# Performance work log

Measured on AMD Instinct MI355X. Metric: run time of the kernel, lower is better.

The kernel has to match this reference:

```python
import jax, jax.numpy as jnp
import numpy as np
import math

BS, SEQ, LQ = 64, 2048, 128
NHEADS, D_TIME, NH, DV = 4, 128, 128, 2
D_K = D_TIME // NHEADS
T10_LO, T10_HI = 0.1, 5.0
M0_LO, M0_HI = 0.1, 10.0
XFA_MAX_DEG = 25.0
REG_H = 200


def setup_inputs() -> dict:
    key = jax.random.key(0)
    ks = jax.random.split(key, 40)
    w = lambda i, shape, s=0.05: jax.random.normal(ks[i], shape, dtype=jnp.float32) * s
    return {
        "X_fa_in": jax.random.uniform(ks[0], (BS, SEQ), dtype=jnp.float32),
        "fa_vals": jax.random.uniform(ks[1], (BS, SEQ), dtype=jnp.float32),
        "fa_mask": jax.random.bernoulli(ks[2], 0.7, (BS, SEQ)),
        "fa_len": jnp.full((BS, 1), float(SEQ), dtype=jnp.float32),
        "TR_vals": jax.random.uniform(ks[3], (BS, SEQ), dtype=jnp.float32),
        "te_lin_w": w(4, (1, 1)), "te_lin_b": w(5, (1,)),
        "te_per_w": w(6, (D_TIME - 1, 1), 1.0), "te_per_b": w(7, (D_TIME - 1,)),
        "q_w": w(8, (D_TIME, D_TIME)), "q_b": w(9, (D_TIME,)),
        "k_w": w(10, (D_TIME, D_TIME)), "k_b": w(11, (D_TIME,)),
        "att_out_w": w(12, (NH, NHEADS * DV)), "att_out_b": w(13, (NH,)),
        "gru_wih": w(14, (3 * NH, NH)), "gru_whh": w(15, (3 * NH, NH)),
        "gru_bih": w(16, (3 * NH,)), "gru_bhh": w(17, (3 * NH,)),
        "score_t10_w": w(18, (1, NH)), "score_m0_w": w(19, (1, NH)),
        "regT_w1": w(20, (REG_H, NH)), "regT_b1": w(21, (REG_H,)),
        "regT_w2": w(22, (REG_H, REG_H)), "regT_b2": w(23, (REG_H,)),
        "regT_w3": w(24, (1, REG_H)), "regT_b3": w(25, (1,)),
        "regM_w1": w(26, (REG_H, NH)), "regM_b1": w(27, (REG_H,)),
        "regM_w2": w(28, (REG_H, REG_H)), "regM_b2": w(29, (REG_H,)),
        "regM_w3": w(30, (1, REG_H)), "regM_b3": w(31, (1,)),
    }


def _time_embed(t, lw, lb, pw, pb):
    # t: (..., L) -> (..., L, D_TIME); linear(1->1) concat sin(linear(1->D_TIME-1))
    t = t[..., None]
    lin = t * lw[0, 0] + lb                      # (..., L, 1)
    per = jnp.sin(t @ pw.T + pb)                 # (..., L, D_TIME-1)
    return jnp.concatenate([lin, per], axis=-1)


def _gru(x, wih, whh, bih, bhh):
    # x: (bs, T, NH) -> (bs, T, NH), torch nn.GRU semantics, h0 = 0
    x_gates = jnp.einsum('bth,gh->btg', x, wih) + bih  # (bs, T, 3*NH)

    def step(h, xt):
        gh = h @ whh.T + bhh
        ri, zi, ni = jnp.split(xt, 3, axis=-1)
        rh, zh, nh = jnp.split(gh, 3, axis=-1)
        r = jax.nn.sigmoid(ri + rh)
        z = jax.nn.sigmoid(zi + zh)
        n = jnp.tanh(ni + r * nh)
        hn = (1.0 - z) * n + z * h
        return hn, hn

    h0 = jnp.zeros((x.shape[0], whh.shape[1]), dtype=x.dtype)
    _, hs = jax.lax.scan(step, h0, x_gates.transpose(1, 0, 2))
    return hs.transpose(1, 0, 2)


def _mlp(h, w1, b1, w2, b2, w3, b3):
    h = jax.nn.gelu(h @ w1.T + b1, approximate=False)
    h = jax.nn.gelu(h @ w2.T + b2, approximate=False)
    return h @ w3.T + b3


def reference(X_fa_in, fa_vals, fa_mask, fa_len, TR_vals,
              te_lin_w, te_lin_b, te_per_w, te_per_b,
              q_w, q_b, k_w, k_b, att_out_w, att_out_b,
              gru_wih, gru_whh, gru_bih, gru_bhh,
              score_t10_w, score_m0_w,
              regT_w1, regT_b1, regT_w2, regT_b2, regT_w3, regT_b3,
              regM_w1, regM_b1, regM_w2, regM_b2, regM_w3, regM_b3):
    bs, seq = X_fa_in.shape
    # ---- time embeddings (dropout inactive / eval) ----
    key_input = fa_vals / math.radians(XFA_MAX_DEG - 1.0)
    k_emb = _time_embed(key_input, te_lin_w, te_lin_b, te_per_w, te_per_b)   # (bs, seq, D_TIME)
    q_ref = jnp.linspace(0.0, 1.0, LQ, dtype=X_fa_in.dtype)[None, :]         # (1, LQ)
    q_emb = _time_embed(q_ref, te_lin_w, te_lin_b, te_per_w, te_per_b)       # (1, LQ, D_TIME)

    # ---- multi-time attention ----
    q = (q_emb @ q_w.T + q_b).reshape(1, LQ, NHEADS, D_K).transpose(0, 2, 1, 3)[0]  # (h, LQ, d_k)
    k = (k_emb @ k_w.T + k_b).reshape(bs, seq, NHEADS, D_K).transpose(0, 2, 1, 3)    # (bs, h, seq, d_k)
    scores = jnp.einsum('hqd,bhsd->bhqs', q, k) / jnp.sqrt(jnp.asarray(D_K, X_fa_in.dtype))
    # mask is broadcast identically across the d_v replication in the original,
    # so the per-channel softmax collapses to one softmax over keys.
    scores = jnp.where(fa_mask[:, None, None, :], scores, jnp.asarray(-1e9, scores.dtype))
    p = jax.nn.softmax(scores, axis=-1)                                      # (bs, h, LQ, seq)
    v = jnp.concatenate([X_fa_in[..., None], fa_mask.astype(X_fa_in.dtype)[..., None]], axis=-1)  # (bs, seq, 2)
    attn = jnp.einsum('bhqs,bsd->bhqd', p, v)                                # (bs, h, LQ, 2)
    concat = attn.transpose(0, 2, 1, 3).reshape(bs, LQ, NHEADS * DV)
    att_out = concat @ att_out_w.T + att_out_b                               # (bs, LQ, NH)

    # ---- GRU + attention pooling ----
    out = _gru(att_out, gru_wih, gru_whh, gru_bih, gru_bhh)                  # (bs, LQ, NH)
    sT = jax.nn.softmax(out @ score_t10_w.T, axis=1)                         # (bs, LQ, 1)
    sM = jax.nn.softmax(out @ score_m0_w.T, axis=1)
    hidden_T10 = jnp.sum(out * sT, axis=1)                                   # (bs, NH)
    hidden_M0 = jnp.sum(out * sM, axis=1)

    T10 = T10_LO + jax.nn.sigmoid(_mlp(hidden_T10, regT_w1, regT_b1, regT_w2, regT_b2, regT_w3, regT_b3)) * (T10_HI - T10_LO)  # (bs, 1)
    M0 = M0_LO + jax.nn.sigmoid(_mlp(hidden_M0, regM_w1, regM_b1, regM_w2, regM_b2, regM_w3, regM_b3)) * (M0_HI - M0_LO)       # (bs, 1)
    R1 = 1.0 / T10
    E = jnp.exp(-TR_vals * R1)                                               # (bs, seq)
    X_out = (1.0 - E) * jnp.sin(fa_vals) / (1.0 - jnp.cos(fa_vals) * E) * M0
    return (X_out, T10, M0)
```

## Files before the change

kernel.cpp:

```cpp
#include <hip/hip_runtime.h>

#define BS 64
#define SEQ 2048
#define LQ 128
#define NH 128

typedef short bf16x8 __attribute__((ext_vector_type(8)));
typedef float f32x4 __attribute__((ext_vector_type(4)));
typedef unsigned short u16x4 __attribute__((ext_vector_type(4)));
typedef unsigned uint2v __attribute__((ext_vector_type(2)));

__device__ __forceinline__ unsigned short f2bf(float f) {
  unsigned u = __float_as_uint(f);
  u = (u + 0x7FFFu + ((u >> 16) & 1u)) >> 16;
  return (unsigned short)u;
}
__device__ __forceinline__ float b2f(unsigned short u) {
  return __uint_as_float((unsigned)u << 16);
}
__device__ __forceinline__ float sigm(float x) { return 1.f / (1.f + __expf(-x)); }
__device__ __forceinline__ float gelu_f(float x) { return 0.5f * x * (1.f + erff(x * 0.70710678118654752f)); }
__device__ __forceinline__ float fexp2(float x) { float y; asm("v_exp_f32 %0, %1" : "=v"(y) : "v"(x)); return y; }
__device__ __forceinline__ float frcp(float x) { float y; asm("v_rcp_f32 %0, %1" : "=v"(y) : "v"(x)); return y; }
__device__ __forceinline__ unsigned cvtpk(float lo, float hi) {
  unsigned d; asm("v_cvt_pk_bf16_f32 %0, %1, %2" : "=v"(d) : "v"(lo), "v"(hi)); return d;
}

__device__ __forceinline__ void softbar() {
  asm volatile("s_waitcnt lgkmcnt(0)" ::: "memory");
  __builtin_amdgcn_s_barrier();
  __builtin_amdgcn_sched_barrier(0);
}

__global__ __launch_bounds__(384) void k_prep(
    const void* __restrict__ mraw,
    const float* __restrict__ qw, const float* __restrict__ qb,
    const float* __restrict__ lw, const float* __restrict__ lb,
    const float* __restrict__ pw, const float* __restrict__ pb,
    const float* __restrict__ wih, const float* __restrict__ bih,
    const float* __restrict__ bhh,
    const float* __restrict__ aow, const float* __restrict__ aob,
    float* __restrict__ maskf, unsigned short* __restrict__ qbf,
    float* __restrict__ fwc) {
  const int tid = threadIdx.x;
  const int blk = blockIdx.x;
  if (blk < 342) {
    __shared__ int sflag;
    if (tid < 64) {
      const unsigned* raw = (const unsigned*)mraw;
      int isf = 0, isb = 0;
#pragma unroll
      for (int k = 0; k < 4; ++k) {
        unsigned w = raw[tid + k * 64];
        isf |= (w == 0x3F800000u);
        isb |= (w > 1u);
      }
      isf = __any(isf);
      isb = __any(isb);
      if (tid == 0) sflag = isf ? 2 : (isb ? 1 : 0);
    }
    __syncthreads();
    int fl = sflag;
    int i = blk * 384 + tid;
    if (i < BS * SEQ) {
      float v;
      if (fl == 2)      v = (((const float*)mraw)[i] != 0.f) ? 1.f : 0.f;
      else if (fl == 1) v = (((const unsigned char*)mraw)[i] != 0) ? 1.f : 0.f;
      else              v = (((const int*)mraw)[i] != 0) ? 1.f : 0.f;
      maskf[i] = v;
    }
  } else if (blk < 350) {
    __shared__ float emb[16 * 132];
    __shared__ float Ac[128], Bc[128];
    const int sb = blk - 342;
    if (tid < 128) {
      Ac[tid] = (tid == 0) ? lw[0] : pw[tid - 1];
      Bc[tid] = (tid == 0) ? lb[0] : pb[tid - 1];
    }
    __syncthreads();
    if (tid < 256) {
      int lq = tid >> 4, e0 = (tid & 15) * 8;
      float tv = (float)(sb * 16 + lq) * (1.f / 127.f);
#pragma unroll
      for (int k = 0; k < 8; ++k) {
        int e = e0 + k;
        float arg = fmaf(tv, Ac[e], Bc[e]);
        emb[lq * 132 + e] = (e == 0) ? arg : __sinf(arg);
      }
    }
    __syncthreads();
    if (tid < 256) {
      const int c = tid & 127, lh = tid >> 7;
      float acc[8];
#pragma unroll
      for (int i = 0; i < 8; ++i) acc[i] = qb[c];
      for (int e4 = 0; e4 < 32; ++e4) {
        float4 wv = *(const float4*)(qw + c * 128 + e4 * 4);
#pragma unroll
        for (int i = 0; i < 8; ++i) {
          const float* er = &emb[(lh * 8 + i) * 132 + e4 * 4];
          acc[i] += wv.x * er[0] + wv.y * er[1] + wv.z * er[2] + wv.w * er[3];
        }
      }
#pragma unroll
      for (int i = 0; i < 8; ++i) {
        int lq = sb * 16 + lh * 8 + i;
        qbf[((c >> 5) * LQ + lq) * 32 + (c & 31)] = f2bf(acc[i]);
      }
    }
  } else {
    const int g = tid;
    const float sc = (g < 256) ? -1.4426950408889634f : 2.8853900817779268f;
    float fw[8];
#pragma unroll
    for (int c = 0; c < 8; ++c) fw[c] = 0.f;
    float cg = bih[g] + (g < 256 ? bhh[g] : 0.f);
    for (int j = 0; j < 128; ++j) {
      float w = wih[g * 128 + j];
      cg = fmaf(w, aob[j], cg);
#pragma unroll
      for (int c = 0; c < 8; ++c) fw[c] = fmaf(w, aow[j * 8 + c], fw[c]);
    }
#pragma unroll
    for (int c = 0; c < 8; ++c) fwc[g * 12 + c] = fw[c] * sc;
    fwc[g * 12 + 8] = cg * sc;
  }
}

__global__ __launch_bounds__(384) void k_xgate(
    const float* __restrict__ fwc, const float* __restrict__ part,
    unsigned short* __restrict__ xg) {
  __shared__ float at[64][8];
  const int tid = threadIdx.x;
  const int t = blockIdx.x;
  if (tid < 256) {
    int b = tid >> 2, h = tid & 3;
    const float* p = part + ((size_t)(b * LQ + t) * 4 + h) * 8;
    float4 p0 = *(const float4*)p;
    float4 p1 = *(const float4*)(p + 4);
    float a = p0.x + p0.z + p1.x + p1.z;
    float l = p0.y + p0.w + p1.y + p1.w;
    at[b][h * 2] = a / l;
    at[b][h * 2 + 1] = 1.f;
  }
  __syncthreads();
  const int q = tid >> 2, s = tid & 3;
  float wv[4][8], cg[4];
#pragma unroll
  for (int j = 0; j < 4; ++j) {
    int row = q * 4 + j;
    float4 a0 = *(const float4*)(fwc + row * 12);
    float4 a1 = *(const float4*)(fwc + row * 12 + 4);
    wv[j][0] = a0.x; wv[j][1] = a0.y; wv[j][2] = a0.z; wv[j][3] = a0.w;
    wv[j][4] = a1.x; wv[j][5] = a1.y; wv[j][6] = a1.z; wv[j][7] = a1.w;
    cg[j] = fwc[row * 12 + 8];
  }
  unsigned short* obase = xg + (((size_t)t * 96 + q) * 64 + s * 16) * 4;
#pragma unroll 4
  for (int bb = 0; bb < 16; ++bb) {
    const float* a = at[s * 16 + bb];
    u16x4 o;
#pragma unroll
    for (int j = 0; j < 4; ++j) {
      float acc = cg[j] + wv[j][0] * a[0] + wv[j][1] * a[1] + wv[j][2] * a[2] + wv[j][3] * a[3]
                        + wv[j][4] * a[4] + wv[j][5] * a[5] + wv[j][6] * a[6] + wv[j][7] * a[7];
      o[j] = f2bf(acc);
    }
    *(u16x4*)(obase + bb * 4) = o;
  }
}

__global__ __launch_bounds__(256) void k_attn(
    const float* __restrict__ Xfa, const float* __restrict__ maskf,
    const float* __restrict__ fav,
    const float* __restrict__ kw, const float* __restrict__ kb,
    const float* __restrict__ lw, const float* __restrict__ lb,
    const float* __restrict__ pw, const float* __restrict__ pb,
    const unsigned short* __restrict__ qbf,
    float* __restrict__ part) {
  __shared__ unsigned short kwl[128 * 136];
  __shared__ unsigned short ktl[64 * 136];
  __shared__ float xt[64], mtl[64], kbl[128], Ac[128], Bc[128];

  const int tid = threadIdx.x;
  const int lane = tid & 63, wave = tid >> 6;
  const int l15 = lane & 15, kg = lane >> 4;
  const int b = blockIdx.x >> 2, qt = blockIdx.x & 3;
  const float KSCALE = 2.3873241463784303f;
  const float C2 = 0.25505654f;

  if (tid < 128) {
    Ac[tid] = (tid == 0) ? lw[0] : pw[tid - 1];
    Bc[tid] = (tid == 0) ? lb[0] : pb[tid - 1];
    kbl[tid] = kb[tid];
  }
  for (int idx = tid; idx < 2048; idx += 256) {
    int d = idx >> 4, e0 = (idx & 15) * 8;
    const float* src = kw + d * 128 + e0;
    float4 s0 = *(const float4*)(src);
    float4 s1 = *(const float4*)(src + 4);
    bf16x8 v;
    v[0] = (short)f2bf(s0.x); v[1] = (short)f2bf(s0.y);
    v[2] = (short)f2bf(s0.z); v[3] = (short)f2bf(s0.w);
    v[4] = (short)f2bf(s1.x); v[5] = (short)f2bf(s1.y);
    v[6] = (short)f2bf(s1.z); v[7] = (short)f2bf(s1.w);
    *(bf16x8*)&kwl[d * 136 + e0] = v;
  }
  bf16x8 qa[4][2];
#pragma unroll
  for (int h = 0; h < 4; ++h)
#pragma unroll
    for (int mt = 0; mt < 2; ++mt) {
      int qrow = (wave * 2 + mt) * 16 + l15;
      qa[h][mt] = *(const bf16x8*)(qbf + (h * 128 + qrow) * 32 + kg * 8);
    }
  float sl[4][2][4], sa[4][2][4];
#pragma unroll
  for (int h = 0; h < 4; ++h)
#pragma unroll
    for (int mt = 0; mt < 2; ++mt)
#pragma unroll
      for (int r = 0; r < 4; ++r) { sl[h][mt][r] = 0.f; sa[h][mt][r] = 0.f; }
  __syncthreads();

  for (int t8 = 0; t8 < 8; ++t8) {
    const int s0 = qt * 512 + t8 * 64;
    bf16x8 af[4];
    {
      float tv = fav[b * SEQ + s0 + wave * 16 + l15] * KSCALE;
#pragma unroll
      for (int kp = 0; kp < 4; ++kp) {
        bf16x8 v;
#pragma unroll
        for (int j = 0; j < 8; ++j) {
          int e = kp * 32 + kg * 8 + j;
          float arg = fmaf(tv, Ac[e], Bc[e]);
          float val = (e == 0) ? arg : __sinf(arg);
          v[j] = (short)f2bf(val);
        }
        af[kp] = v;
      }
      if (tid < 64) {
        xt[tid] = Xfa[b * SEQ + s0 + tid];
        mtl[tid] = maskf[b * SEQ + s0 + tid];
      }
    }
#pragma unroll
    for (int h = 0; h < 4; ++h) {
#pragma unroll
      for (int nt = 0; nt < 2; ++nt) {
        f32x4 acc = {0.f, 0.f, 0.f, 0.f};
#pragma unroll
        for (int kp = 0; kp < 4; ++kp) {
          bf16x8 bb = *(const bf16x8*)&kwl[(h * 32 + nt * 16 + l15) * 136 + kp * 32 + kg * 8];
          acc = __builtin_amdgcn_mfma_f32_16x16x32_bf16(af[kp], bb, acc, 0, 0, 0);
        }
        int d = nt * 16 + l15;
        float kbv = kbl[h * 32 + d];
#pragma unroll
        for (int r = 0; r < 4; ++r) {
          int srow = wave * 16 + kg * 4 + r;
          ktl[srow * 136 + h * 32 + d] = f2bf(acc[r] + kbv);
        }
      }
    }
    softbar();
    {
      float xv[4], mv[4];
#pragma unroll
      for (int nt2 = 0; nt2 < 4; ++nt2) {
        int scol = nt2 * 16 + l15;
        xv[nt2] = xt[scol];
        mv[nt2] = mtl[scol];
      }
#pragma unroll
      for (int h = 0; h < 4; ++h) {
        f32x4 D[2][4];
#pragma unroll
        for (int nt2 = 0; nt2 < 4; ++nt2) {
          int scol = nt2 * 16 + l15;
          bf16x8 bk = *(const bf16x8*)&ktl[scol * 136 + h * 32 + kg * 8];
#pragma unroll
          for (int mt = 0; mt < 2; ++mt) {
            f32x4 z = {0.f, 0.f, 0.f, 0.f};
            D[mt][nt2] = __builtin_amdgcn_mfma_f32_16x16x32_bf16(qa[h][mt], bk, z, 0, 0, 0);
          }
        }
#pragma unroll
        for (int mt = 0; mt < 2; ++mt)
#pragma unroll
          for (int r = 0; r < 4; ++r) {
            float p0 = mv[0] * exp2f(D[mt][0][r] * C2);
            float p1 = mv[1] * exp2f(D[mt][1][r] * C2);
            float p2 = mv[2] * exp2f(D[mt][2][r] * C2);
            float p3 = mv[3] * exp2f(D[mt][3][r] * C2);
            sl[h][mt][r] += (p0 + p1) + (p2 + p3);
            sa[h][mt][r] += fmaf(p0, xv[0], fmaf(p1, xv[1], fmaf(p2, xv[2], p3 * xv[3])));
          }
      }
    }
    softbar();
  }
#pragma unroll
  for (int h = 0; h < 4; ++h)
#pragma unroll
    for (int mt = 0; mt < 2; ++mt)
#pragma unroll
      for (int r = 0; r < 4; ++r) {
        float l = sl[h][mt][r], a = sa[h][mt][r];
#pragma unroll
        for (int off = 1; off <= 8; off <<= 1) {
          l += __shfl_xor(l, off);
          a += __shfl_xor(a, off);
        }
        if (l15 == 0) {
          int q = (wave * 2 + mt) * 16 + kg * 4 + r;
          float* p = part + ((size_t)(b * LQ + q) * 4 + h) * 8 + qt * 2;
          p[0] = a;
          p[1] = l;
        }
      }
}

__global__ __launch_bounds__(512) void k_gru8(
    const float* __restrict__ whh, const float* __restrict__ bhh,
    const unsigned short* __restrict__ xg, unsigned short* __restrict__ gout) {
  __shared__ unsigned short hbf[2][16][132];
  const int tid = threadIdx.x;
  const int lane = tid & 63, w = tid >> 6;
  const int l15 = lane & 15, kg = lane >> 4;
  const int b0 = blockIdx.x * 16;

  for (int i = tid; i < 2 * 16 * 132 / 2; i += 512) ((unsigned*)hbf)[i] = 0u;

  bf16x8 wfr[3][4];
#pragma unroll
  for (int n = 0; n < 3; ++n) {
    const float sc = (n < 2) ? -1.4426950408889634f : 2.8853900817779268f;
    const float* wrow = whh + (n * 128 + w * 16 + l15) * 128 + kg * 8;
#pragma unroll
    for (int kk = 0; kk < 4; ++kk) {
      float4 f0 = *(const float4*)(wrow + kk * 32);
      float4 f1 = *(const float4*)(wrow + kk * 32 + 4);
      bf16x8 v;
      v[0] = (short)f2bf(f0.x * sc); v[1] = (short)f2bf(f0.y * sc);
      v[2] = (short)f2bf(f0.z * sc); v[3] = (short)f2bf(f0.w * sc);
      v[4] = (short)f2bf(f1.x * sc); v[5] = (short)f2bf(f1.y * sc);
      v[6] = (short)f2bf(f1.z * sc); v[7] = (short)f2bf(f1.w * sc);
      wfr[n][kk] = v;
    }
  }
  float bhn[4];
  {
    float4 t = *(const float4*)(bhh + 256 + w * 16 + kg * 4);
    bhn[0] = t.x * 2.8853900817779268f; bhn[1] = t.y * 2.8853900817779268f;
    bhn[2] = t.z * 2.8853900817779268f; bhn[3] = t.w * 2.8853900817779268f;
  }
  float hold[4] = {0.f, 0.f, 0.f, 0.f};

  const unsigned short* xlane = xg + (((size_t)(w * 4 + kg)) * 64 + b0 + l15) * 4;
  unsigned short* gptr = gout + (size_t)(b0 + l15) * LQ * NH + w * 16 + kg * 4;

  u16x4 xA[2][3], xB[2][3];
#pragma unroll
  for (int s = 0; s < 2; ++s)
#pragma unroll
    for (int n = 0; n < 3; ++n)
      xA[s][n] = *(const u16x4*)(xlane + (size_t)s * 24576 + n * 8192);
  __syncthreads();

#define GRU_STEP(T, XQ)                                                                 \
  {                                                                                     \
    const int t_ = (T);                                                                 \
    bf16x8 hf[4];                                                                       \
    _Pragma("unroll")                                                                   \
    for (int kk = 0; kk < 4; ++kk)                                                      \
      hf[kk] = *(const bf16x8*)&hbf[t_ & 1][l15][kg * 8 + kk * 32];                     \
    f32x4 acc[3];                                                                       \
    _Pragma("unroll")                                                                   \
    for (int n = 0; n < 3; ++n) {                                                       \
      f32x4 z = {0.f, 0.f, 0.f, 0.f};                                                   \
      f32x4 p = __builtin_amdgcn_mfma_f32_16x16x32_bf16(wfr[n][0], hf[0], z, 0, 0, 0);  \
      p = __builtin_amdgcn_mfma_f32_16x16x32_bf16(wfr[n][1], hf[1], p, 0, 0, 0);        \
      f32x4 q = __builtin_amdgcn_mfma_f32_16x16x32_bf16(wfr[n][2], hf[2], z, 0, 0, 0);  \
      q = __builtin_amdgcn_mfma_f32_16x16x32_bf16(wfr[n][3], hf[3], q, 0, 0, 0);        \
      acc[n] = p + q;                                                                   \
    }                                                                                   \
    float hv[4];                                                                        \
    _Pragma("unroll")                                                                   \
    for (int r = 0; r < 4; ++r) {                                                       \
      float R = frcp(1.f + fexp2(acc[0][r] + b2f(XQ[0][r])));                           \
      float Z = frcp(1.f + fexp2(acc[1][r] + b2f(XQ[1][r])));                           \
      float u = fmaf(R, acc[2][r] + bhn[r], b2f(XQ[2][r]));                             \
      float Tt = frcp(1.f + fexp2(u));                                                  \
      float ng = fmaf(-2.f, Tt, 1.f);                                                   \
      float hn = fmaf(Z, hold[r] - ng, ng);                                             \
      hold[r] = hn;                                                                     \
      hv[r] = hn;                                                                       \
    }                                                                                   \
    uint2v d;                                                                           \
    d[0] = cvtpk(hv[0], hv[1]);                                                         \
    d[1] = cvtpk(hv[2], hv[3]);                                                         \
    *(uint2v*)&hbf[(t_ & 1) ^ 1][l15][w * 16 + kg * 4] = d;                             \
    *(uint2v*)(gptr + (size_t)t_ * NH) = d;                                             \
    softbar();                                                                          \
  }

#define GRU_PAIR(TP, XC, XN)                                                            \
  {                                                                                     \
    const int tp_ = (TP);                                                               \
    const int tl = (tp_ < 63) ? (tp_ + 1) : 63;                                         \
    _Pragma("unroll")                                                                   \
    for (int s = 0; s < 2; ++s)                                                         \
      _Pragma("unroll")                                                                 \
      for (int n = 0; n < 3; ++n)                                                       \
        XN[s][n] = *(const u16x4*)(xlane + ((size_t)(tl * 2 + s)) * 24576 + n * 8192);  \
    GRU_STEP(tp_ * 2, XC[0]);                                                           \
    GRU_STEP(tp_ * 2 + 1, XC[1]);                                                       \
  }

#pragma unroll 1
  for (int tp = 0; tp < 64; tp += 2) {
    GRU_PAIR(tp, xA, xB);
    GRU_PAIR(tp + 1, xB, xA);
  }
#undef GRU_PAIR
#undef GRU_STEP
}

__global__ __launch_bounds__(256) void k_heads(
    const unsigned short* __restrict__ gout,
    const float* __restrict__ swT, const float* __restrict__ swM,
    const float* __restrict__ tw1, const float* __restrict__ tb1,
    const float* __restrict__ tw2, const float* __restrict__ tb2,
    const float* __restrict__ tw3, const float* __restrict__ tb3,
    const float* __restrict__ mw1, const float* __restrict__ mb1,
    const float* __restrict__ mw2, const float* __restrict__ mb2,
    const float* __restrict__ mw3, const float* __restrict__ mb3,
    const float* __restrict__ fav, const float* __restrict__ TRv,
    float* __restrict__ out) {
  __shared__ float hbuf[128 * 129];
  __shared__ float lT[128], lM[128], pT[128], pM[128];
  __shared__ float hidT[128], hidM[128];
  __shared__ float l1b[200], l2b[200];
  __shared__ float parts[4];
  __shared__ float scal[2];
  const int tid = threadIdx.x;
  const int b = blockIdx.x;
  for (int rep = 0; rep < 64; ++rep) {
    int i = rep * 256 + tid;
    hbuf[(i >> 7) * 129 + (i & 127)] = b2f(gout[(size_t)b * (LQ * NH) + i]);
  }
  __syncthreads();
  if (tid < 128) {
    float aT = 0.f, aM = 0.f;
    for (int j = 0; j < 128; ++j) {
      float v = hbuf[tid * 129 + j];
      aT = fmaf(v, swT[j], aT);
      aM = fmaf(v, swM[j], aM);
    }
    lT[tid] = aT; lM[tid] = aM;
  }
  __syncthreads();
  if (tid < 64) {
    float v0 = lT[tid], v1 = lT[tid + 64];
    float m = fmaxf(v0, v1);
    for (int off = 32; off > 0; off >>= 1) m = fmaxf(m, __shfl_xor(m, off));
    float p0 = __expf(v0 - m), p1 = __expf(v1 - m);
    float s = p0 + p1;
    for (int off = 32; off > 0; off >>= 1) s += __shfl_xor(s, off);
    float inv = 1.f / s;
    pT[tid] = p0 * inv; pT[tid + 64] = p1 * inv;
  } else if (tid < 128) {
    int l = tid - 64;
    float v0 = lM[l], v1 = lM[l + 64];
    float m = fmaxf(v0, v1);
    for (int off = 32; off > 0; off >>= 1) m = fmaxf(m, __shfl_xor(m, off));
    float p0 = __expf(v0 - m), p1 = __expf(v1 - m);
    float s = p0 + p1;
    for (int off = 32; off > 0; off >>= 1) s += __shfl_xor(s, off);
    float inv = 1.f / s;
    pM[l] = p0 * inv; pM[l + 64] = p1 * inv;
  }
  __syncthreads();
  if (tid < 128) {
    float aT = 0.f, aM = 0.f;
    for (int t = 0; t < 128; ++t) {
      float v = hbuf[t * 129 + tid];
      aT = fmaf(v, pT[t], aT);
      aM = fmaf(v, pM[t], aM);
    }
    hidT[tid] = aT; hidM[tid] = aM;
  }
  __syncthreads();
#pragma unroll 1
  for (int hd = 0; hd < 2; ++hd) {
    const float* in = hd ? hidM : hidT;
    const float* w1 = hd ? mw1 : tw1; const float* b1 = hd ? mb1 : tb1;
    const float* w2 = hd ? mw2 : tw2; const float* b2 = hd ? mb2 : tb2;
    const float* w3 = hd ? mw3 : tw3; const float* b3 = hd ? mb3 : tb3;
    if (tid < 200) {
      float acc = b1[tid];
      for (int j4 = 0; j4 < 32; ++j4) {
        float4 wv = *(const float4*)(w1 + tid * 128 + j4 * 4);
        acc += wv.x * in[j4 * 4] + wv.y * in[j4 * 4 + 1] + wv.z * in[j4 * 4 + 2] + wv.w * in[j4 * 4 + 3];
      }
      l1b[tid] = gelu_f(acc);
    }
    __syncthreads();
    if (tid < 200) {
      float acc = b2[tid];
      for (int k4 = 0; k4 < 50; ++k4) {
        float4 wv = *(const float4*)(w2 + tid * 200 + k4 * 4);
        acc += wv.x * l1b[k4 * 4] + wv.y * l1b[k4 * 4 + 1] + wv.z * l1b[k4 * 4 + 2] + wv.w * l1b[k4 * 4 + 3];
      }
      l2b[tid] = gelu_f(acc);
    }
    __syncthreads();
    float part = (tid < 200) ? l2b[tid] * w3[tid] : 0.f;
    for (int off = 32; off > 0; off >>= 1) part += __shfl_xor(part, off);
    if ((tid & 63) == 0) parts[tid >> 6] = part;
    __syncthreads();
    if (tid == 0) {
      float y = parts[0] + parts[1] + parts[2] + parts[3] + b3[0];
      float hi = hd ? 10.f : 5.f;
      float val = 0.1f + sigm(y) * (hi - 0.1f);
      scal[hd] = val;
      out[BS * SEQ + hd * BS + b] = val;
    }
    __syncthreads();
  }
  float T10 = scal[0], M0 = scal[1];
  float R1 = 1.f / T10;
  for (int i = tid; i < SEQ; i += 256) {
    float fa = fav[b * SEQ + i];
    float tr = TRv[b * SEQ + i];
    float E = __expf(-tr * R1);
    float s, c;
    __sincosf(fa, &s, &c);
    out[b * SEQ + i] = (1.f - E) * s / (1.f - c * E) * M0;
  }
}

extern "C" void kernel_launch(void* const* d_in, const int* in_sizes, int n_in,
                              void* d_out, int out_size, void* d_ws, size_t ws_size,
                              hipStream_t stream) {
  const float* Xfa = (const float*)d_in[0];
  const float* fav = (const float*)d_in[1];
  const void*  mraw = d_in[2];
  const float* TRv = (const float*)d_in[4];
  const float* lw = (const float*)d_in[5];
  const float* lb = (const float*)d_in[6];
  const float* pw = (const float*)d_in[7];
  const float* pb = (const float*)d_in[8];
  const float* qw = (const float*)d_in[9];
  const float* qb = (const float*)d_in[10];
  const float* kw = (const float*)d_in[11];
  const float* kb = (const float*)d_in[12];
  const float* aow = (const float*)d_in[13];
  const float* aob = (const float*)d_in[14];
  const float* wih = (const float*)d_in[15];
  const float* whh = (const float*)d_in[16];
  const float* bih = (const float*)d_in[17];
  const float* bhh = (const float*)d_in[18];
  const float* swT = (const float*)d_in[19];
  const float* swM = (const float*)d_in[20];
  const float* tw1 = (const float*)d_in[21];
  const float* tb1 = (const float*)d_in[22];
  const float* tw2 = (const float*)d_in[23];
  const float* tb2 = (const float*)d_in[24];
  const float* tw3 = (const float*)d_in[25];
  const float* tb3 = (const float*)d_in[26];
  const float* mw1 = (const float*)d_in[27];
  const float* mb1 = (const float*)d_in[28];
  const float* mw2 = (const float*)d_in[29];
  const float* mb2 = (const float*)d_in[30];
  const float* mw3 = (const float*)d_in[31];
  const float* mb3 = (const float*)d_in[32];
  float* out = (float*)d_out;
  char* ws = (char*)d_ws;

  unsigned short* qbf = (unsigned short*)ws;
  float* part = (float*)(ws + 32768);
  unsigned short* gout = (unsigned short*)(ws + 32768);
  float* fwc = (float*)(ws + 2129920);
  float* maskf = (float*)(ws + 2148352);
  unsigned short* xgate = (unsigned short*)(ws + 2672768);

  k_prep<<<351, 384, 0, stream>>>(mraw, qw, qb, lw, lb, pw, pb,
                                  wih, bih, bhh, aow, aob, maskf, qbf, fwc);
  k_attn<<<256, 256, 0, stream>>>(Xfa, maskf, fav, kw, kb, lw, lb, pw, pb, qbf, part);
  k_xgate<<<128, 384, 0, stream>>>(fwc, part, xgate);
  k_gru8<<<4, 512, 0, stream>>>(whh, bhh, xgate, gout);
  k_heads<<<64, 256, 0, stream>>>(gout, swT, swM, tw1, tb1, tw2, tb2, tw3, tb3,
                                  mw1, mb1, mw2, mb2, mw3, mb3, fav, TRv, out);
}
```

Measured before the change: 188.4 us.

## Double-buffer attention K tiles, fold mask/scale into logits, tweak GRU and heads

The attention kernel now double-buffers the key tile, mask and X tiles in shared memory. It computes the next stage's K projection before the barrier instead of after it, which removes one barrier per iteration. The mask becomes an additive bias of 0 or -30000 and the softmax scale is folded into Q when it is prepared, so the inner loop runs a raw v_exp_f32 with no multiplies. The GRU step starts its MFMA accumulators from the x-gate and bias terms, dropping post-adds. The heads kernel uses vectorized bf16 loads and splits its reductions across all 256 threads. The double buffering raises LDS use in k_attn, which may lower occupancy.

```diff
diff --git a/kernel.cpp b/kernel.cpp
--- a/kernel.cpp
+++ b/kernel.cpp
@@ -40,7 +40,7 @@
     const float* __restrict__ wih, const float* __restrict__ bih,
     const float* __restrict__ bhh,
     const float* __restrict__ aow, const float* __restrict__ aob,
-    float* __restrict__ maskf, unsigned short* __restrict__ qbf,
+    float* __restrict__ maskb, unsigned short* __restrict__ qbf,
     float* __restrict__ fwc) {
   const int tid = threadIdx.x;
   const int blk = blockIdx.x;
@@ -63,16 +63,17 @@
     int fl = sflag;
     int i = blk * 384 + tid;
     if (i < BS * SEQ) {
-      float v;
-      if (fl == 2)      v = (((const float*)mraw)[i] != 0.f) ? 1.f : 0.f;
-      else if (fl == 1) v = (((const unsigned char*)mraw)[i] != 0) ? 1.f : 0.f;
-      else              v = (((const int*)mraw)[i] != 0) ? 1.f : 0.f;
-      maskf[i] = v;
+      bool on;
+      if (fl == 2)      on = (((const float*)mraw)[i] != 0.f);
+      else if (fl == 1) on = (((const unsigned char*)mraw)[i] != 0);
+      else              on = (((const int*)mraw)[i] != 0);
+      maskb[i] = on ? 0.f : -30000.f;
     }
   } else if (blk < 350) {
     __shared__ float emb[16 * 132];
     __shared__ float Ac[128], Bc[128];
     const int sb = blk - 342;
+    const float C2 = 0.25505654f;
     if (tid < 128) {
       Ac[tid] = (tid == 0) ? lw[0] : pw[tid - 1];
       Bc[tid] = (tid == 0) ? lb[0] : pb[tid - 1];
@@ -105,7 +106,7 @@
 #pragma unroll
       for (int i = 0; i < 8; ++i) {
         int lq = sb * 16 + lh * 8 + i;
-        qbf[((c >> 5) * LQ + lq) * 32 + (c & 31)] = f2bf(acc[i]);
+        qbf[((c >> 5) * LQ + lq) * 32 + (c & 31)] = f2bf(acc[i] * C2);
       }
     }
   } else {
@@ -171,7 +172,7 @@
 }
 
 __global__ __launch_bounds__(256) void k_attn(
-    const float* __restrict__ Xfa, const float* __restrict__ maskf,
+    const float* __restrict__ Xfa, const float* __restrict__ maskb,
     const float* __restrict__ fav,
     const float* __restrict__ kw, const float* __restrict__ kb,
     const float* __restrict__ lw, const float* __restrict__ lb,
@@ -179,15 +180,14 @@
     const unsigned short* __restrict__ qbf,
     float* __restrict__ part) {
   __shared__ unsigned short kwl[128 * 136];
-  __shared__ unsigned short ktl[64 * 136];
-  __shared__ float xt[64], mtl[64], kbl[128], Ac[128], Bc[128];
+  __shared__ unsigned short ktl[2][64 * 136];
+  __shared__ float xt[2][64], mtl[2][64], kbl[128], Ac[128], Bc[128];
 
   const int tid = threadIdx.x;
   const int lane = tid & 63, wave = tid >> 6;
   const int l15 = lane & 15, kg = lane >> 4;
   const int b = blockIdx.x >> 2, qt = blockIdx.x & 3;
   const float KSCALE = 2.3873241463784303f;
-  const float C2 = 0.25505654f;
 
   if (tid < 128) {
     Ac[tid] = (tid == 0) ? lw[0] : pw[tid - 1];
@@ -223,55 +223,66 @@
       for (int r = 0; r < 4; ++r) { sl[h][mt][r] = 0.f; sa[h][mt][r] = 0.f; }
   __syncthreads();
 
+#define ATTN_STAGE(TT)                                                                   \
+  {                                                                                      \
+    const int tt_ = (TT);                                                                \
+    const int ss0 = qt * 512 + tt_ * 64;                                                 \
+    float tv = fav[b * SEQ + ss0 + wave * 16 + l15] * KSCALE;                            \
+    float xfv = 0.f, mbv = 0.f;                                                          \
+    if (tid < 64) {                                                                      \
+      xfv = Xfa[b * SEQ + ss0 + tid];                                                    \
+      mbv = maskb[b * SEQ + ss0 + tid];                                                  \
+    }                                                                                    \
+    bf16x8 af[4];                                                                        \
+    _Pragma("unroll")                                                                    \
+    for (int kp = 0; kp < 4; ++kp) {                                                     \
+      bf16x8 v;                                                                          \
+      _Pragma("unroll")                                                                  \
+      for (int j = 0; j < 8; ++j) {                                                      \
+        int e = kp * 32 + kg * 8 + j;                                                    \
+        float arg = fmaf(tv, Ac[e], Bc[e]);                                              \
+        float val = (e == 0) ? arg : __sinf(arg);                                        \
+        v[j] = (short)f2bf(val);                                                         \
+      }                                                                                  \
+      af[kp] = v;                                                                        \
+    }                                                                                    \
+    _Pragma("unroll")                                                                    \
+    for (int h = 0; h < 4; ++h) {                                                        \
+      _Pragma("unroll")                                                                  \
+      for (int nt = 0; nt < 2; ++nt) {                                                   \
+        f32x4 acc = {0.f, 0.f, 0.f, 0.f};                                                \
+        _Pragma("unroll")                                                                \
+        for (int kp = 0; kp < 4; ++kp) {                                                 \
+          bf16x8 bb = *(const bf16x8*)&kwl[(h * 32 + nt * 16 + l15) * 136 + kp * 32 + kg * 8]; \
+          acc = __builtin_amdgcn_mfma_f32_16x16x32_bf16(af[kp], bb, acc, 0, 0, 0);       \
+        }                                                                                \
+        int d = nt * 16 + l15;                                                           \
+        float kbv = kbl[h * 32 + d];                                                     \
+        _Pragma("unroll")                                                                \
+        for (int r = 0; r < 4; ++r) {                                                    \
+          int srow = wave * 16 + kg * 4 + r;                                             \
+          ktl[tt_ & 1][srow * 136 + h * 32 + d] = f2bf(acc[r] + kbv);                    \
+        }                                                                                \
+      }                                                                                  \
+    }                                                                                    \
+    if (tid < 64) {                                                                      \
+      xt[tt_ & 1][tid] = xfv;                                                            \
+      mtl[tt_ & 1][tid] = mbv;                                                           \
+    }                                                                                    \
+  }
+
+  ATTN_STAGE(0);
+  softbar();
+#pragma unroll 1
   for (int t8 = 0; t8 < 8; ++t8) {
-    const int s0 = qt * 512 + t8 * 64;
-    bf16x8 af[4];
-    {
-      float tv = fav[b * SEQ + s0 + wave * 16 + l15] * KSCALE;
-#pragma unroll
-      for (int kp = 0; kp < 4; ++kp) {
-        bf16x8 v;
-#pragma unroll
-        for (int j = 0; j < 8; ++j) {
-          int e = kp * 32 + kg * 8 + j;
-          float arg = fmaf(tv, Ac[e], Bc[e]);
-          float val = (e == 0) ? arg : __sinf(arg);
-          v[j] = (short)f2bf(val);
-        }
-        af[kp] = v;
-      }
-      if (tid < 64) {
-        xt[tid] = Xfa[b * SEQ + s0 + tid];
-        mtl[tid] = maskf[b * SEQ + s0 + tid];
-      }
-    }
-#pragma unroll
-    for (int h = 0; h < 4; ++h) {
-#pragma unroll
-      for (int nt = 0; nt < 2; ++nt) {
-        f32x4 acc = {0.f, 0.f, 0.f, 0.f};
-#pragma unroll
-        for (int kp = 0; kp < 4; ++kp) {
-          bf16x8 bb = *(const bf16x8*)&kwl[(h * 32 + nt * 16 + l15) * 136 + kp * 32 + kg * 8];
-          acc = __builtin_amdgcn_mfma_f32_16x16x32_bf16(af[kp], bb, acc, 0, 0, 0);
-        }
-        int d = nt * 16 + l15;
-        float kbv = kbl[h * 32 + d];
-#pragma unroll
-        for (int r = 0; r < 4; ++r) {
-          int srow = wave * 16 + kg * 4 + r;
-          ktl[srow * 136 + h * 32 + d] = f2bf(acc[r] + kbv);
-        }
-      }
-    }
-    softbar();
+    const int cur = t8 & 1;
     {
       float xv[4], mv[4];
 #pragma unroll
       for (int nt2 = 0; nt2 < 4; ++nt2) {
         int scol = nt2 * 16 + l15;
-        xv[nt2] = xt[scol];
-        mv[nt2] = mtl[scol];
+        xv[nt2] = xt[cur][scol];
+        mv[nt2] = mtl[cur][scol];
       }
 #pragma unroll
       for (int h = 0; h < 4; ++h) {
@@ -279,7 +290,7 @@
 #pragma unroll
         for (int nt2 = 0; nt2 < 4; ++nt2) {
           int scol = nt2 * 16 + l15;
-          bf16x8 bk = *(const bf16x8*)&ktl[scol * 136 + h * 32 + kg * 8];
+          bf16x8 bk = *(const bf16x8*)&ktl[cur][scol * 136 + h * 32 + kg * 8];
 #pragma unroll
           for (int mt = 0; mt < 2; ++mt) {
             f32x4 z = {0.f, 0.f, 0.f, 0.f};
@@ -290,17 +301,19 @@
         for (int mt = 0; mt < 2; ++mt)
 #pragma unroll
           for (int r = 0; r < 4; ++r) {
-            float p0 = mv[0] * exp2f(D[mt][0][r] * C2);
-            float p1 = mv[1] * exp2f(D[mt][1][r] * C2);
-            float p2 = mv[2] * exp2f(D[mt][2][r] * C2);
-            float p3 = mv[3] * exp2f(D[mt][3][r] * C2);
+            float p0 = fexp2(D[mt][0][r] + mv[0]);
+            float p1 = fexp2(D[mt][1][r] + mv[1]);
+            float p2 = fexp2(D[mt][2][r] + mv[2]);
+            float p3 = fexp2(D[mt][3][r] + mv[3]);
             sl[h][mt][r] += (p0 + p1) + (p2 + p3);
             sa[h][mt][r] += fmaf(p0, xv[0], fmaf(p1, xv[1], fmaf(p2, xv[2], p3 * xv[3])));
           }
       }
     }
+    if (t8 < 7) ATTN_STAGE(t8 + 1);
     softbar();
   }
+#undef ATTN_STAGE
 #pragma unroll
   for (int h = 0; h < 4; ++h)
 #pragma unroll
@@ -322,7 +335,7 @@
       }
 }
 
-__global__ __launch_bounds__(512) void k_gru8(
+__global__ __launch_bounds__(512) void k_gru9(
     const float* __restrict__ whh, const float* __restrict__ bhh,
     const unsigned short* __restrict__ xg, unsigned short* __restrict__ gout) {
   __shared__ unsigned short hbf[2][16][132];
@@ -350,11 +363,11 @@
       wfr[n][kk] = v;
     }
   }
-  float bhn[4];
+  f32x4 bhnv;
   {
     float4 t = *(const float4*)(bhh + 256 + w * 16 + kg * 4);
-    bhn[0] = t.x * 2.8853900817779268f; bhn[1] = t.y * 2.8853900817779268f;
-    bhn[2] = t.z * 2.8853900817779268f; bhn[3] = t.w * 2.8853900817779268f;
+    bhnv[0] = t.x * 2.8853900817779268f; bhnv[1] = t.y * 2.8853900817779268f;
+    bhnv[2] = t.z * 2.8853900817779268f; bhnv[3] = t.w * 2.8853900817779268f;
   }
   float hold[4] = {0.f, 0.f, 0.f, 0.f};
 
@@ -376,22 +389,29 @@
     _Pragma("unroll")                                                                   \
     for (int kk = 0; kk < 4; ++kk)                                                      \
       hf[kk] = *(const bf16x8*)&hbf[t_ & 1][l15][kg * 8 + kk * 32];                     \
-    f32x4 acc[3];                                                                       \
+    f32x4 c0, c1;                                                                       \
     _Pragma("unroll")                                                                   \
-    for (int n = 0; n < 3; ++n) {                                                       \
-      f32x4 z = {0.f, 0.f, 0.f, 0.f};                                                   \
-      f32x4 p = __builtin_amdgcn_mfma_f32_16x16x32_bf16(wfr[n][0], hf[0], z, 0, 0, 0);  \
-      p = __builtin_amdgcn_mfma_f32_16x16x32_bf16(wfr[n][1], hf[1], p, 0, 0, 0);        \
-      f32x4 q = __builtin_amdgcn_mfma_f32_16x16x32_bf16(wfr[n][2], hf[2], z, 0, 0, 0);  \
-      q = __builtin_amdgcn_mfma_f32_16x16x32_bf16(wfr[n][3], hf[3], q, 0, 0, 0);        \
-      acc[n] = p + q;                                                                   \
-    }                                                                                   \
+    for (int r = 0; r < 4; ++r) { c0[r] = b2f(XQ[0][r]); c1[r] = b2f(XQ[1][r]); }       \
+    f32x4 z4 = {0.f, 0.f, 0.f, 0.f};                                                    \
+    f32x4 p0 = __builtin_amdgcn_mfma_f32_16x16x32_bf16(wfr[0][0], hf[0], c0, 0, 0, 0);  \
+    p0 = __builtin_amdgcn_mfma_f32_16x16x32_bf16(wfr[0][1], hf[1], p0, 0, 0, 0);        \
+    f32x4 q0 = __builtin_amdgcn_mfma_f32_16x16x32_bf16(wfr[0][2], hf[2], z4, 0, 0, 0);  \
+    q0 = __builtin_amdgcn_mfma_f32_16x16x32_bf16(wfr[0][3], hf[3], q0, 0, 0, 0);        \
+    f32x4 p1 = __builtin_amdgcn_mfma_f32_16x16x32_bf16(wfr[1][0], hf[0], c1, 0, 0, 0);  \
+    p1 = __builtin_amdgcn_mfma_f32_16x16x32_bf16(wfr[1][1], hf[1], p1, 0, 0, 0);        \
+    f32x4 q1 = __builtin_amdgcn_mfma_f32_16x16x32_bf16(wfr[1][2], hf[2], z4, 0, 0, 0);  \
+    q1 = __builtin_amdgcn_mfma_f32_16x16x32_bf16(wfr[1][3], hf[3], q1, 0, 0, 0);        \
+    f32x4 p2 = __builtin_amdgcn_mfma_f32_16x16x32_bf16(wfr[2][0], hf[0], bhnv, 0, 0, 0);\
+    p2 = __builtin_amdgcn_mfma_f32_16x16x32_bf16(wfr[2][1], hf[1], p2, 0, 0, 0);        \
+    f32x4 q2 = __builtin_amdgcn_mfma_f32_16x16x32_bf16(wfr[2][2], hf[2], z4, 0, 0, 0);  \
+    q2 = __builtin_amdgcn_mfma_f32_16x16x32_bf16(wfr[2][3], hf[3], q2, 0, 0, 0);        \
+    f32x4 a0 = p0 + q0, a1 = p1 + q1, a2 = p2 + q2;                                     \
     float hv[4];                                                                        \
     _Pragma("unroll")                                                                   \
     for (int r = 0; r < 4; ++r) {                                                       \
-      float R = frcp(1.f + fexp2(acc[0][r] + b2f(XQ[0][r])));                           \
-      float Z = frcp(1.f + fexp2(acc[1][r] + b2f(XQ[1][r])));                           \
-      float u = fmaf(R, acc[2][r] + bhn[r], b2f(XQ[2][r]));                             \
+      float R = frcp(1.f + fexp2(a0[r]));                                               \
+      float Z = frcp(1.f + fexp2(a1[r]));                                               \
+      float u = fmaf(R, a2[r], b2f(XQ[2][r]));                                          \
       float Tt = frcp(1.f + fexp2(u));                                                  \
       float ng = fmaf(-2.f, Tt, 1.f);                                                   \
       float hn = fmaf(Z, hold[r] - ng, ng);                                             \
@@ -440,30 +460,39 @@
     const float* __restrict__ fav, const float* __restrict__ TRv,
     float* __restrict__ out) {
   __shared__ float hbuf[128 * 129];
-  __shared__ float lT[128], lM[128], pT[128], pM[128];
+  __shared__ float pp[2][128][2];
+  __shared__ float pT[128], pM[128];
   __shared__ float hidT[128], hidM[128];
   __shared__ float l1b[200], l2b[200];
   __shared__ float parts[4];
   __shared__ float scal[2];
   const int tid = threadIdx.x;
   const int b = blockIdx.x;
-  for (int rep = 0; rep < 64; ++rep) {
-    int i = rep * 256 + tid;
-    hbuf[(i >> 7) * 129 + (i & 127)] = b2f(gout[(size_t)b * (LQ * NH) + i]);
-  }
-  __syncthreads();
-  if (tid < 128) {
+#pragma unroll
+  for (int rep = 0; rep < 8; ++rep) {
+    int idx = rep * 2048 + tid * 8;
+    int row = idx >> 7, col = idx & 127;
+    bf16x8 v = *(const bf16x8*)(gout + (size_t)b * (LQ * NH) + idx);
+#pragma unroll
+    for (int j = 0; j < 8; ++j)
+      hbuf[row * 129 + col + j] = b2f((unsigned short)v[j]);
+  }
+  __syncthreads();
+  {
+    int t = tid & 127, hf2 = tid >> 7;
     float aT = 0.f, aM = 0.f;
-    for (int j = 0; j < 128; ++j) {
-      float v = hbuf[tid * 129 + j];
-      aT = fmaf(v, swT[j], aT);
-      aM = fmaf(v, swM[j], aM);
-    }
-    lT[tid] = aT; lM[tid] = aM;
+    for (int j = 0; j < 64; ++j) {
+      float v = hbuf[t * 129 + hf2 * 64 + j];
+      aT = fmaf(v, swT[hf2 * 64 + j], aT);
+      aM = fmaf(v, swM[hf2 * 64 + j], aM);
+    }
+    pp[hf2][t][0] = aT;
+    pp[hf2][t][1] = aM;
   }
   __syncthreads();
   if (tid < 64) {
-    float v0 = lT[tid], v1 = lT[tid + 64];
+    float v0 = pp[0][tid][0] + pp[1][tid][0];
+    float v1 = pp[0][tid + 64][0] + pp[1][tid + 64][0];
     float m = fmaxf(v0, v1);
     for (int off = 32; off > 0; off >>= 1) m = fmaxf(m, __shfl_xor(m, off));
     float p0 = __expf(v0 - m), p1 = __expf(v1 - m);
@@ -473,7 +502,8 @@
     pT[tid] = p0 * inv; pT[tid + 64] = p1 * inv;
   } else if (tid < 128) {
     int l = tid - 64;
-    float v0 = lM[l], v1 = lM[l + 64];
+    float v0 = pp[0][l][1] + pp[1][l][1];
+    float v1 = pp[0][l + 64][1] + pp[1][l + 64][1];
     float m = fmaxf(v0, v1);
     for (int off = 32; off > 0; off >>= 1) m = fmaxf(m, __shfl_xor(m, off));
     float p0 = __expf(v0 - m), p1 = __expf(v1 - m);
@@ -483,14 +513,22 @@
     pM[l] = p0 * inv; pM[l + 64] = p1 * inv;
   }
   __syncthreads();
-  if (tid < 128) {
+  {
+    int j = tid & 127, hf2 = tid >> 7;
     float aT = 0.f, aM = 0.f;
-    for (int t = 0; t < 128; ++t) {
-      float v = hbuf[t * 129 + tid];
+    for (int t2 = 0; t2 < 64; ++t2) {
+      int t = hf2 * 64 + t2;
+      float v = hbuf[t * 129 + j];
       aT = fmaf(v, pT[t], aT);
       aM = fmaf(v, pM[t], aM);
     }
-    hidT[tid] = aT; hidM[tid] = aM;
+    pp[hf2][j][0] = aT;
+    pp[hf2][j][1] = aM;
+  }
+  __syncthreads();
+  if (tid < 128) {
+    hidT[tid] = pp[0][tid][0] + pp[1][tid][0];
+    hidM[tid] = pp[0][tid][1] + pp[1][tid][1];
   }
   __syncthreads();
 #pragma unroll 1
@@ -584,14 +622,14 @@
   float* part = (float*)(ws + 32768);
   unsigned short* gout = (unsigned short*)(ws + 32768);
   float* fwc = (float*)(ws + 2129920);
-  float* maskf = (float*)(ws + 2148352);
+  float* maskb = (float*)(ws + 2148352);
   unsigned short* xgate = (unsigned short*)(ws + 2672768);
 
   k_prep<<<351, 384, 0, stream>>>(mraw, qw, qb, lw, lb, pw, pb,
-                                  wih, bih, bhh, aow, aob, maskf, qbf, fwc);
-  k_attn<<<256, 256, 0, stream>>>(Xfa, maskf, fav, kw, kb, lw, lb, pw, pb, qbf, part);
+                                  wih, bih, bhh, aow, aob, maskb, qbf, fwc);
+  k_attn<<<256, 256, 0, stream>>>(Xfa, maskb, fav, kw, kb, lw, lb, pw, pb, qbf, part);
   k_xgate<<<128, 384, 0, stream>>>(fwc, part, xgate);
-  k_gru8<<<4, 512, 0, stream>>>(whh, bhh, xgate, gout);
+  k_gru9<<<4, 512, 0, stream>>>(whh, bhh, xgate, gout);
   k_heads<<<64, 256, 0, stream>>>(gout, swT, swM, tw1, tb1, tw2, tb2, tw3, tb3,
                                   mw1, mb1, mw2, mb2, mw3, mb3, fav, TRv, out);
 }
```

New measurement: 178.6 us. 1.05x faster.
